# Optimization experiments

Hardware: AMD Instinct MI355X
Metric: run time of the kernel (lower is better)

## Reference

```python
import jax, jax.numpy as jnp
import numpy as np

B, S, F, OWN, H, E = 16384, 37, 17, 9, 256, 128
NOUT = 7 + 16


def setup_inputs() -> dict:
    key = jax.random.key(0)
    ks = jax.random.split(key, 22)
    obs = jax.random.normal(ks[0], (B, S + 1, F), dtype=jnp.float32)
    pad = jax.random.bernoulli(ks[1], 0.3, (B, S))
    obs = obs.at[:, 1:, :].multiply(jnp.where(pad, 0.0, 1.0)[:, :, None])

    def init(k, shape):
        return jax.random.normal(k, shape, dtype=jnp.float32) * 0.05

    params = dict(
        sW1=init(ks[2], (F, H)), sb1=jnp.zeros((H,), jnp.float32),
        sW2=init(ks[3], (H, H)), sb2=jnp.zeros((H,), jnp.float32),
        sW3=init(ks[4], (H, E)), sb3=jnp.zeros((E,), jnp.float32),
        aW1=init(ks[5], (E + OWN, H)), ab1=jnp.zeros((H,), jnp.float32),
        aW2=init(ks[6], (H, H)), ab2=jnp.zeros((H,), jnp.float32),
        aW3=init(ks[7], (H, NOUT)), ab3=jnp.zeros((NOUT,), jnp.float32),
        vW1=init(ks[8], (E + OWN, H)), vb1=jnp.zeros((H,), jnp.float32),
        vW2=init(ks[9], (H, H)), vb2=jnp.zeros((H,), jnp.float32),
        vW3=init(ks[10], (H, 1)), vb3=jnp.zeros((1,), jnp.float32),
    )
    return {"obs": obs, **params}


def reference(obs, sW1, sb1, sW2, sb2, sW3, sb3,
              aW1, ab1, aW2, ab2, aW3, ab3,
              vW1, vb1, vW2, vb2, vW3, vb3):
    s_own = obs[:, 0, :OWN]                      # [B, 9]
    seqs = obs[:, 1:, :]                         # [B, 37, 17]
    # non-padded mask: rows whose abs-sum is nonzero
    mask = (jnp.sum(jnp.abs(seqs), axis=-1) != 0).astype(obs.dtype)  # [B, 37]

    # shared MLP applied to every row; masked positions zeroed before the
    # pooling sum (equivalent to gather->MLP->scatter into zeros->sum)
    h = jax.nn.relu(seqs @ sW1 + sb1)
    h = jax.nn.relu(h @ sW2 + sb2)
    h = jax.nn.relu(h @ sW3 + sb3)               # [B, 37, E]
    h = h * mask[..., None]
    summed = jnp.sum(h, axis=1)                  # [B, E]

    cat = jnp.concatenate([summed, s_own], axis=1)  # [B, E+9]

    a = jax.nn.relu(cat @ aW1 + ab1)
    a = jax.nn.relu(a @ aW2 + ab2)
    action_logits = a @ aW3 + ab3                # [B, 23]

    v = jax.nn.relu(cat @ vW1 + vb1)
    v = jax.nn.relu(v @ vW2 + vb2)
    value = (v @ vW3 + vb3).reshape(-1)          # [B]

    return action_logits, value
```

## Files before the change

### kernel.cpp

```cpp
#include <hip/hip_runtime.h>
#include <hip/hip_bf16.h>

#define B_    16384
#define S_    37
#define F_    17
#define OWN_  9
#define NOUT_ 23
#define OBS_ROW 646

typedef __bf16 bf16x8 __attribute__((ext_vector_type(8)));
typedef __bf16 bf16x4 __attribute__((ext_vector_type(4)));
typedef float  f32x4  __attribute__((ext_vector_type(4)));

#define MFMA(a,b,c) __builtin_amdgcn_mfma_f32_16x16x32_bf16(a, b, c, 0, 0, 0)

#define W1F_OFF   0
#define W2F_OFF   8192
#define W3F_OFF   73728
#define AW1F_OFF  106496
#define AW2F_OFF  147456
#define AW3F_OFF  212992
#define VW1F_OFF  221184
#define VW2F_OFF  262144
#define VW3F_OFF  327680
#define PREP_TOTAL 331776

__global__ void prep_kernel(const float* __restrict__ sW1, const float* __restrict__ sW2,
                            const float* __restrict__ sW3, const float* __restrict__ aW1,
                            const float* __restrict__ aW2, const float* __restrict__ aW3,
                            const float* __restrict__ vW1, const float* __restrict__ vW2,
                            const float* __restrict__ vW3, __bf16* __restrict__ ws)
{
    int j = blockIdx.x * 256 + threadIdx.x;
    const float* src; __bf16* dst; int Np, Ks, Ns;
    if (j < 8192)                  { dst = ws + W1F_OFF;  src = sW1; Np = 256; Ks = 17;  Ns = 256; }
    else if ((j -= 8192)  < 65536) { dst = ws + W2F_OFF;  src = sW2; Np = 256; Ks = 256; Ns = 256; }
    else if ((j -= 65536) < 32768) { dst = ws + W3F_OFF;  src = sW3; Np = 128; Ks = 256; Ns = 128; }
    else if ((j -= 32768) < 40960) { dst = ws + AW1F_OFF; src = aW1; Np = 256; Ks = 137; Ns = 256; }
    else if ((j -= 40960) < 65536) { dst = ws + AW2F_OFF; src = aW2; Np = 256; Ks = 256; Ns = 256; }
    else if ((j -= 65536) < 8192)  { dst = ws + AW3F_OFF; src = aW3; Np = 32;  Ks = 256; Ns = 23;  }
    else if ((j -= 8192)  < 40960) { dst = ws + VW1F_OFF; src = vW1; Np = 256; Ks = 137; Ns = 256; }
    else if ((j -= 40960) < 65536) { dst = ws + VW2F_OFF; src = vW2; Np = 256; Ks = 256; Ns = 256; }
    else { j -= 65536;               dst = ws + VW3F_OFF; src = vW3; Np = 16;  Ks = 256; Ns = 1;   }
    const int c = j / (Np * 8), rem = j - c * Np * 8, n = rem >> 3, e = rem & 7, k = c * 8 + e;
    const float v = (k < Ks && n < Ns) ? src[k * Ns + n] : 0.f;
    dst[j] = (__bf16)v;
}

__global__ __launch_bounds__(512, 2) void fused_kernel(
    const float* __restrict__ obs,
    const float* __restrict__ sb1, const float* __restrict__ sb2, const float* __restrict__ sb3,
    const float* __restrict__ ab1, const float* __restrict__ ab2, const float* __restrict__ ab3,
    const float* __restrict__ vb1, const float* __restrict__ vb2, const float* __restrict__ vb3,
    const __bf16* __restrict__ ws, float* __restrict__ out)
{
    __shared__ __align__(16) char pool[109056];
    __bf16* act1    = (__bf16*)pool;
    __bf16* act2    = (__bf16*)(pool + 32768);
    __bf16* xs_full = (__bf16*)(pool + 65536);
    float*  sm_full = (float*)(pool + 106496);
    __bf16* catf    = (__bf16*)(pool + 65536);
    float*  partial = (float*)pool;

    const __bf16* W1f  = ws + W1F_OFF;
    const __bf16* W2f  = ws + W2F_OFF;
    const __bf16* W3f  = ws + W3F_OFF;
    const __bf16* AW1f = ws + AW1F_OFF;
    const __bf16* AW2f = ws + AW2F_OFF;
    const __bf16* AW3f = ws + AW3F_OFF;
    const __bf16* VW1f = ws + VW1F_OFF;
    const __bf16* VW2f = ws + VW2F_OFF;
    const __bf16* VW3f = ws + VW3F_OFF;

    const int tid  = threadIdx.x;
    const int wave = tid >> 6;
    const int lane = tid & 63;
    const int q    = lane >> 4;
    const int l16  = lane & 15;
    const int qh   = q >> 1;
    const int e4   = (q & 1) * 4;
    const int b0   = blockIdx.x * 16;
    const int nc   = wave & 3;
    const int mr   = wave >> 2;
    const f32x4 z4 = {0.f, 0.f, 0.f, 0.f};

    #pragma unroll
    for (int i = 0; i < 5; ++i)
        ((f32x4*)xs_full)[tid + i * 512] = z4;

    bf16x8 w1f[2], w2f[8][2], w3f[2][8];
    f32x4 b1q[2], b2q[2], b3q[2];
    #pragma unroll
    for (int nt = 0; nt < 2; ++nt) {
        const int n = wave * 32 + nt * 16 + l16;
        w1f[nt] = *(const bf16x8*)(W1f + ((size_t)q * 256 + n) * 8);
        b1q[nt] = *(const f32x4*)(sb1 + wave * 32 + nt * 16 + q * 4);
        b2q[nt] = *(const f32x4*)(sb2 + wave * 32 + nt * 16 + q * 4);
        b3q[nt] = *(const f32x4*)(sb3 + nc * 32 + nt * 16 + q * 4);
        #pragma unroll
        for (int k = 0; k < 8; ++k) {
            w2f[k][nt] = *(const bf16x8*)(W2f + ((size_t)(k * 4 + q) * 256 + n) * 8);
            w3f[nt][k] = *(const bf16x8*)(W3f + ((size_t)(k * 4 + q) * 128 + nc * 32 + nt * 16 + l16) * 8);
        }
    }

    __syncthreads();

    for (int rr = tid; rr < 640; rr += 512) {
        const int g = rr >> 6, tr = rr & 63, b = tr & 15, sl = tr >> 4;
        const int s = g * 4 + sl;
        float sm = 0.f;
        if (s < S_) {
            const float* p = obs + (size_t)(b0 + b) * OBS_ROW + (s + 1) * F_;
            #pragma unroll
            for (int c = 0; c < F_; ++c) {
                const float v = p[c];
                sm += fabsf(v);
                xs_full[g * 2048 + ((c >> 3) * 64 + tr) * 8 + (c & 7)] = (__bf16)v;
            }
        }
        sm_full[rr] = sm;
    }

    __syncthreads();

    f32x4 vsum[2] = {z4, z4};

    for (int it = 0; it < 10; ++it) {
        const __bf16* xg  = xs_full + it * 2048;
        const float*  smg = sm_full + it * 64;

        #pragma unroll
        for (int m = 0; m < 4; ++m) {
            const bf16x8 xm = *(const bf16x8*)(xg + (q * 64 + m * 16 + l16) * 8);
            #pragma unroll
            for (int nt = 0; nt < 2; ++nt) {
                const f32x4 h = MFMA(w1f[nt], xm, z4);
                float v0 = h[0] + b1q[nt][0]; v0 = v0 > 0.f ? v0 : 0.f;
                float v1 = h[1] + b1q[nt][1]; v1 = v1 > 0.f ? v1 : 0.f;
                float v2 = h[2] + b1q[nt][2]; v2 = v2 > 0.f ? v2 : 0.f;
                float v3 = h[3] + b1q[nt][3]; v3 = v3 > 0.f ? v3 : 0.f;
                const bf16x4 pk = {(__bf16)v0, (__bf16)v1, (__bf16)v2, (__bf16)v3};
                *(bf16x4*)(act1 + ((wave * 4 + nt * 2 + qh) * 64 + m * 16 + l16) * 8 + e4) = pk;
            }
        }
        __syncthreads();

        {
            f32x4 h2[2][4];
            #pragma unroll
            for (int nt = 0; nt < 2; ++nt)
                #pragma unroll
                for (int m = 0; m < 4; ++m) h2[nt][m] = z4;
            #pragma unroll
            for (int k = 0; k < 8; ++k) {
                const int k8 = k * 4 + q;
                #pragma unroll
                for (int m = 0; m < 4; ++m) {
                    const bf16x8 a = *(const bf16x8*)(act1 + (k8 * 64 + m * 16 + l16) * 8);
                    h2[0][m] = MFMA(w2f[k][0], a, h2[0][m]);
                    h2[1][m] = MFMA(w2f[k][1], a, h2[1][m]);
                }
            }
            #pragma unroll
            for (int nt = 0; nt < 2; ++nt)
                #pragma unroll
                for (int m = 0; m < 4; ++m) {
                    float v0 = h2[nt][m][0] + b2q[nt][0]; v0 = v0 > 0.f ? v0 : 0.f;
                    float v1 = h2[nt][m][1] + b2q[nt][1]; v1 = v1 > 0.f ? v1 : 0.f;
                    float v2 = h2[nt][m][2] + b2q[nt][2]; v2 = v2 > 0.f ? v2 : 0.f;
                    float v3 = h2[nt][m][3] + b2q[nt][3]; v3 = v3 > 0.f ? v3 : 0.f;
                    const bf16x4 pk = {(__bf16)v0, (__bf16)v1, (__bf16)v2, (__bf16)v3};
                    *(bf16x4*)(act2 + ((wave * 4 + nt * 2 + qh) * 64 + m * 16 + l16) * 8 + e4) = pk;
                }
        }
        __syncthreads();

        {
            f32x4 h3[2][2] = {{z4, z4}, {z4, z4}};
            #pragma unroll
            for (int k = 0; k < 8; ++k) {
                const int k8 = k * 4 + q;
                #pragma unroll
                for (int mi = 0; mi < 2; ++mi) {
                    const bf16x8 a = *(const bf16x8*)(act2 + (k8 * 64 + (mr * 2 + mi) * 16 + l16) * 8);
                    h3[0][mi] = MFMA(w3f[0][k], a, h3[0][mi]);
                    h3[1][mi] = MFMA(w3f[1][k], a, h3[1][mi]);
                }
            }
            #pragma unroll
            for (int mi = 0; mi < 2; ++mi) {
                const float mk = (smg[(mr * 2 + mi) * 16 + l16] != 0.f) ? 1.f : 0.f;
                #pragma unroll
                for (int nt = 0; nt < 2; ++nt)
                    #pragma unroll
                    for (int r = 0; r < 4; ++r) {
                        float v = h3[nt][mi][r] + b3q[nt][r];
                        v = v > 0.f ? v : 0.f;
                        vsum[nt][r] += mk * v;
                    }
            }
        }
    }

    if (mr == 0) {
        #pragma unroll
        for (int nt = 0; nt < 2; ++nt)
            #pragma unroll
            for (int r = 0; r < 4; ++r)
                partial[(nc * 32 + nt * 16 + q * 4 + r) * 16 + l16] = vsum[nt][r];
    }
    if (tid < 16) {
        const float* p = obs + (size_t)(b0 + tid) * OBS_ROW;
        #pragma unroll
        for (int c = 0; c < 8; ++c) catf[(16 * 16 + tid) * 8 + c] = (__bf16)p[c];
        catf[(17 * 16 + tid) * 8 + 0] = (__bf16)p[8];
        #pragma unroll
        for (int c = 1; c < 8; ++c) catf[(17 * 16 + tid) * 8 + c] = (__bf16)0.f;
    } else if (tid < 32) {
        const int rr = tid - 16;
        #pragma unroll
        for (int c = 0; c < 8; ++c) {
            catf[(18 * 16 + rr) * 8 + c] = (__bf16)0.f;
            catf[(19 * 16 + rr) * 8 + c] = (__bf16)0.f;
        }
    }
    __syncthreads();

    if (mr == 1) {
        #pragma unroll
        for (int nt = 0; nt < 2; ++nt) {
            f32x4 t = vsum[nt];
            #pragma unroll
            for (int r = 0; r < 4; ++r)
                t[r] += partial[(nc * 32 + nt * 16 + q * 4 + r) * 16 + l16];
            const bf16x4 pk = {(__bf16)t[0], (__bf16)t[1], (__bf16)t[2], (__bf16)t[3]};
            *(bf16x4*)(catf + ((nc * 4 + nt * 2 + qh) * 16 + l16) * 8 + e4) = pk;
        }
    }
    __syncthreads();

    {
        f32x4 ha[2] = {z4, z4}, hv[2] = {z4, z4};
        #pragma unroll
        for (int k = 0; k < 5; ++k) {
            const int k8 = k * 4 + q;
            const bf16x8 ca = *(const bf16x8*)(catf + (k8 * 16 + l16) * 8);
            #pragma unroll
            for (int nt = 0; nt < 2; ++nt) {
                const int n = wave * 32 + nt * 16 + l16;
                const bf16x8 ba = *(const bf16x8*)(AW1f + ((size_t)k8 * 256 + n) * 8);
                const bf16x8 bv = *(const bf16x8*)(VW1f + ((size_t)k8 * 256 + n) * 8);
                ha[nt] = MFMA(ba, ca, ha[nt]);
                hv[nt] = MFMA(bv, ca, hv[nt]);
            }
        }
        #pragma unroll
        for (int nt = 0; nt < 2; ++nt) {
            const f32x4 ab_ = *(const f32x4*)(ab1 + wave * 32 + nt * 16 + q * 4);
            const f32x4 vb_ = *(const f32x4*)(vb1 + wave * 32 + nt * 16 + q * 4);
            float a0 = ha[nt][0] + ab_[0]; a0 = a0 > 0.f ? a0 : 0.f;
            float a1 = ha[nt][1] + ab_[1]; a1 = a1 > 0.f ? a1 : 0.f;
            float a2 = ha[nt][2] + ab_[2]; a2 = a2 > 0.f ? a2 : 0.f;
            float a3 = ha[nt][3] + ab_[3]; a3 = a3 > 0.f ? a3 : 0.f;
            float u0 = hv[nt][0] + vb_[0]; u0 = u0 > 0.f ? u0 : 0.f;
            float u1 = hv[nt][1] + vb_[1]; u1 = u1 > 0.f ? u1 : 0.f;
            float u2 = hv[nt][2] + vb_[2]; u2 = u2 > 0.f ? u2 : 0.f;
            float u3 = hv[nt][3] + vb_[3]; u3 = u3 > 0.f ? u3 : 0.f;
            const bf16x4 pa = {(__bf16)a0, (__bf16)a1, (__bf16)a2, (__bf16)a3};
            const bf16x4 pv = {(__bf16)u0, (__bf16)u1, (__bf16)u2, (__bf16)u3};
            const int c = wave * 4 + nt * 2 + qh;
            *(bf16x4*)(act1 + (c * 64 + l16) * 8 + e4)      = pa;
            *(bf16x4*)(act1 + (c * 64 + 16 + l16) * 8 + e4) = pv;
        }
    }
    __syncthreads();

    {
        f32x4 ha[2] = {z4, z4}, hv[2] = {z4, z4};
        #pragma unroll
        for (int k = 0; k < 8; ++k) {
            const int k8 = k * 4 + q;
            const bf16x8 a0 = *(const bf16x8*)(act1 + (k8 * 64 + l16) * 8);
            const bf16x8 a1 = *(const bf16x8*)(act1 + (k8 * 64 + 16 + l16) * 8);
            #pragma unroll
            for (int nt = 0; nt < 2; ++nt) {
                const int n = wave * 32 + nt * 16 + l16;
                const bf16x8 ba = *(const bf16x8*)(AW2f + ((size_t)k8 * 256 + n) * 8);
                const bf16x8 bv = *(const bf16x8*)(VW2f + ((size_t)k8 * 256 + n) * 8);
                ha[nt] = MFMA(ba, a0, ha[nt]);
                hv[nt] = MFMA(bv, a1, hv[nt]);
            }
        }
        #pragma unroll
        for (int nt = 0; nt < 2; ++nt) {
            const f32x4 ab_ = *(const f32x4*)(ab2 + wave * 32 + nt * 16 + q * 4);
            const f32x4 vb_ = *(const f32x4*)(vb2 + wave * 32 + nt * 16 + q * 4);
            float a0 = ha[nt][0] + ab_[0]; a0 = a0 > 0.f ? a0 : 0.f;
            float a1 = ha[nt][1] + ab_[1]; a1 = a1 > 0.f ? a1 : 0.f;
            float a2 = ha[nt][2] + ab_[2]; a2 = a2 > 0.f ? a2 : 0.f;
            float a3 = ha[nt][3] + ab_[3]; a3 = a3 > 0.f ? a3 : 0.f;
            float u0 = hv[nt][0] + vb_[0]; u0 = u0 > 0.f ? u0 : 0.f;
            float u1 = hv[nt][1] + vb_[1]; u1 = u1 > 0.f ? u1 : 0.f;
            float u2 = hv[nt][2] + vb_[2]; u2 = u2 > 0.f ? u2 : 0.f;
            float u3 = hv[nt][3] + vb_[3]; u3 = u3 > 0.f ? u3 : 0.f;
            const bf16x4 pa = {(__bf16)a0, (__bf16)a1, (__bf16)a2, (__bf16)a3};
            const bf16x4 pv = {(__bf16)u0, (__bf16)u1, (__bf16)u2, (__bf16)u3};
            const int c = wave * 4 + nt * 2 + qh;
            *(bf16x4*)(act2 + (c * 64 + l16) * 8 + e4)      = pa;
            *(bf16x4*)(act2 + (c * 64 + 16 + l16) * 8 + e4) = pv;
        }
    }
    __syncthreads();

    if (wave < 2) {
        f32x4 acc = z4;
        #pragma unroll
        for (int k = 0; k < 8; ++k) {
            const int k8 = k * 4 + q;
            const bf16x8 a0 = *(const bf16x8*)(act2 + (k8 * 64 + l16) * 8);
            const bf16x8 bf = *(const bf16x8*)(AW3f + ((size_t)k8 * 32 + wave * 16 + l16) * 8);
            acc = MFMA(bf, a0, acc);
        }
        const int nb = wave * 16 + q * 4;
        #pragma unroll
        for (int r = 0; r < 4; ++r) {
            const int n = nb + r;
            if (n < NOUT_)
                out[(size_t)(b0 + l16) * NOUT_ + n] = acc[r] + ab3[n];
        }
    } else if (wave == 2) {
        f32x4 acc = z4;
        #pragma unroll
        for (int k = 0; k < 8; ++k) {
            const int k8 = k * 4 + q;
            const bf16x8 a1 = *(const bf16x8*)(act2 + (k8 * 64 + 16 + l16) * 8);
            const bf16x8 bf = *(const bf16x8*)(VW3f + ((size_t)k8 * 16 + l16) * 8);
            acc = MFMA(bf, a1, acc);
        }
        if (q == 0)
            out[(size_t)B_ * NOUT_ + b0 + l16] = acc[0] + vb3[0];
    }
}

extern "C" void kernel_launch(void* const* d_in, const int* in_sizes, int n_in,
                              void* d_out, int out_size, void* d_ws, size_t ws_size,
                              hipStream_t stream)
{
    const float* obs = (const float*)d_in[0];
    const float* sW1 = (const float*)d_in[1];
    const float* sb1 = (const float*)d_in[2];
    const float* sW2 = (const float*)d_in[3];
    const float* sb2 = (const float*)d_in[4];
    const float* sW3 = (const float*)d_in[5];
    const float* sb3 = (const float*)d_in[6];
    const float* aW1 = (const float*)d_in[7];
    const float* ab1 = (const float*)d_in[8];
    const float* aW2 = (const float*)d_in[9];
    const float* ab2 = (const float*)d_in[10];
    const float* aW3 = (const float*)d_in[11];
    const float* ab3 = (const float*)d_in[12];
    const float* vW1 = (const float*)d_in[13];
    const float* vb1 = (const float*)d_in[14];
    const float* vW2 = (const float*)d_in[15];
    const float* vb2 = (const float*)d_in[16];
    const float* vW3 = (const float*)d_in[17];
    const float* vb3 = (const float*)d_in[18];

    __bf16* ws = (__bf16*)d_ws;
    float* out = (float*)d_out;

    hipLaunchKernelGGL(prep_kernel, dim3(PREP_TOTAL / 256), dim3(256), 0, stream,
                       sW1, sW2, sW3, aW1, aW2, aW3, vW1, vW2, vW3, ws);
    hipLaunchKernelGGL(fused_kernel, dim3(B_ / 16), dim3(512), 0, stream,
                       obs, sb1, sb2, sb3, ab1, ab2, ab3, vb1, vb2, vb3,
                       (const __bf16*)ws, out);
}
```

Measured before the change: 265.8 us.

## Double-buffer obs staging with 128-row tiles and vectorize weight prep

The sequence loop now handles 128 rows (8 slots × 16 batch) per iteration in 5 iterations instead of 64 rows in 10. The next tile's obs values are loaded into registers before the layer-1 MFMAs and written to a second LDS buffer after the first barrier, so global loads overlap compute and the up-front staging of the whole sequence goes away. Obs reads are spread over 4 threads per row, with a shuffle reduction for the padding mask. The prep kernel now writes packed bf16x8 per thread. LDS use grows to about 145 KB, which may limit how many 512-thread blocks fit per CU despite launch_bounds(512,2).

Result: slower. 349.3 us (+31.4%).

```diff
diff --git a/kernel.cpp b/kernel.cpp
--- a/kernel.cpp
+++ b/kernel.cpp
@@ -23,7 +23,7 @@
 #define VW1F_OFF  221184
 #define VW2F_OFF  262144
 #define VW3F_OFF  327680
-#define PREP_TOTAL 331776
+#define PREP_TOTAL8 41472
 
 __global__ void prep_kernel(const float* __restrict__ sW1, const float* __restrict__ sW2,
                             const float* __restrict__ sW3, const float* __restrict__ aW1,
@@ -31,20 +31,26 @@
                             const float* __restrict__ vW1, const float* __restrict__ vW2,
                             const float* __restrict__ vW3, __bf16* __restrict__ ws)
 {
-    int j = blockIdx.x * 256 + threadIdx.x;
+    int j8 = blockIdx.x * 256 + threadIdx.x;
     const float* src; __bf16* dst; int Np, Ks, Ns;
-    if (j < 8192)                  { dst = ws + W1F_OFF;  src = sW1; Np = 256; Ks = 17;  Ns = 256; }
-    else if ((j -= 8192)  < 65536) { dst = ws + W2F_OFF;  src = sW2; Np = 256; Ks = 256; Ns = 256; }
-    else if ((j -= 65536) < 32768) { dst = ws + W3F_OFF;  src = sW3; Np = 128; Ks = 256; Ns = 128; }
-    else if ((j -= 32768) < 40960) { dst = ws + AW1F_OFF; src = aW1; Np = 256; Ks = 137; Ns = 256; }
-    else if ((j -= 40960) < 65536) { dst = ws + AW2F_OFF; src = aW2; Np = 256; Ks = 256; Ns = 256; }
-    else if ((j -= 65536) < 8192)  { dst = ws + AW3F_OFF; src = aW3; Np = 32;  Ks = 256; Ns = 23;  }
-    else if ((j -= 8192)  < 40960) { dst = ws + VW1F_OFF; src = vW1; Np = 256; Ks = 137; Ns = 256; }
-    else if ((j -= 40960) < 65536) { dst = ws + VW2F_OFF; src = vW2; Np = 256; Ks = 256; Ns = 256; }
-    else { j -= 65536;               dst = ws + VW3F_OFF; src = vW3; Np = 16;  Ks = 256; Ns = 1;   }
-    const int c = j / (Np * 8), rem = j - c * Np * 8, n = rem >> 3, e = rem & 7, k = c * 8 + e;
-    const float v = (k < Ks && n < Ns) ? src[k * Ns + n] : 0.f;
-    dst[j] = (__bf16)v;
+    if (j8 < 1024)                { dst = ws + W1F_OFF;  src = sW1; Np = 256; Ks = 17;  Ns = 256; }
+    else if ((j8 -= 1024) < 8192) { dst = ws + W2F_OFF;  src = sW2; Np = 256; Ks = 256; Ns = 256; }
+    else if ((j8 -= 8192) < 4096) { dst = ws + W3F_OFF;  src = sW3; Np = 128; Ks = 256; Ns = 128; }
+    else if ((j8 -= 4096) < 5120) { dst = ws + AW1F_OFF; src = aW1; Np = 256; Ks = 137; Ns = 256; }
+    else if ((j8 -= 5120) < 8192) { dst = ws + AW2F_OFF; src = aW2; Np = 256; Ks = 256; Ns = 256; }
+    else if ((j8 -= 8192) < 1024) { dst = ws + AW3F_OFF; src = aW3; Np = 32;  Ks = 256; Ns = 23;  }
+    else if ((j8 -= 1024) < 5120) { dst = ws + VW1F_OFF; src = vW1; Np = 256; Ks = 137; Ns = 256; }
+    else if ((j8 -= 5120) < 8192) { dst = ws + VW2F_OFF; src = vW2; Np = 256; Ks = 256; Ns = 256; }
+    else { j8 -= 8192;              dst = ws + VW3F_OFF; src = vW3; Np = 16;  Ks = 256; Ns = 1;   }
+    const int c = j8 / Np, n = j8 - c * Np;
+    bf16x8 pk;
+    #pragma unroll
+    for (int e = 0; e < 8; ++e) {
+        const int k = c * 8 + e;
+        const float v = (k < Ks && n < Ns) ? src[k * Ns + n] : 0.f;
+        pk[e] = (__bf16)v;
+    }
+    *(bf16x8*)(dst + (size_t)j8 * 8) = pk;
 }
 
 __global__ __launch_bounds__(512, 2) void fused_kernel(
@@ -54,12 +60,14 @@
     const float* __restrict__ vb1, const float* __restrict__ vb2, const float* __restrict__ vb3,
     const __bf16* __restrict__ ws, float* __restrict__ out)
 {
-    __shared__ __align__(16) char pool[109056];
-    __bf16* act1    = (__bf16*)pool;
-    __bf16* act2    = (__bf16*)(pool + 32768);
-    __bf16* xs_full = (__bf16*)(pool + 65536);
-    float*  sm_full = (float*)(pool + 106496);
-    __bf16* catf    = (__bf16*)(pool + 65536);
+    __shared__ __align__(16) char pool[148480];
+    __bf16* act1 = (__bf16*)pool;
+    __bf16* act2 = (__bf16*)(pool + 65536);
+    __bf16* xs0  = (__bf16*)(pool + 131072);
+    __bf16* xs1  = (__bf16*)(pool + 139264);
+    float*  sm0  = (float*)(pool + 147456);
+    float*  sm1  = (float*)(pool + 147968);
+    __bf16* catf = (__bf16*)(pool + 131072);
     float*  partial = (float*)pool;
 
     const __bf16* W1f  = ws + W1F_OFF;
@@ -84,9 +92,16 @@
     const int mr   = wave >> 2;
     const f32x4 z4 = {0.f, 0.f, 0.f, 0.f};
 
+    const int sr  = tid >> 2;
+    const int sp  = tid & 3;
+    const int sb  = sr & 15;
+    const int ssl = sr >> 4;
+    const int nf  = (sp == 3) ? 5 : 4;
+    const float* obs_row = obs + (size_t)(b0 + sb) * OBS_ROW;
+
     #pragma unroll
-    for (int i = 0; i < 5; ++i)
-        ((f32x4*)xs_full)[tid + i * 512] = z4;
+    for (int i = 0; i < 2; ++i)
+        ((f32x4*)xs0)[tid + i * 512] = z4;
 
     bf16x8 w1f[2], w2f[8][2], w3f[2][8];
     f32x4 b1q[2], b2q[2], b3q[2];
@@ -106,33 +121,45 @@
 
     __syncthreads();
 
-    for (int rr = tid; rr < 640; rr += 512) {
-        const int g = rr >> 6, tr = rr & 63, b = tr & 15, sl = tr >> 4;
-        const int s = g * 4 + sl;
-        float sm = 0.f;
-        if (s < S_) {
-            const float* p = obs + (size_t)(b0 + b) * OBS_ROW + (s + 1) * F_;
-            #pragma unroll
-            for (int c = 0; c < F_; ++c) {
-                const float v = p[c];
-                sm += fabsf(v);
-                xs_full[g * 2048 + ((c >> 3) * 64 + tr) * 8 + (c & 7)] = (__bf16)v;
-            }
-        }
-        sm_full[rr] = sm;
-    }
-
+    {
+        const float* p = obs_row + (ssl + 1) * F_ + sp * 4;
+        float psum = 0.f;
+        #pragma unroll
+        for (int f = 0; f < 5; ++f) {
+            if (f < nf) {
+                const float v = p[f];
+                psum += fabsf(v);
+                const int c = sp * 4 + f;
+                xs0[((c >> 3) * 128 + sr) * 8 + (c & 7)] = (__bf16)v;
+            }
+        }
+        psum += __shfl_xor(psum, 1);
+        psum += __shfl_xor(psum, 2);
+        if (sp == 0) sm0[sr] = psum;
+    }
     __syncthreads();
 
     f32x4 vsum[2] = {z4, z4};
 
-    for (int it = 0; it < 10; ++it) {
-        const __bf16* xg  = xs_full + it * 2048;
-        const float*  smg = sm_full + it * 64;
-
-        #pragma unroll
-        for (int m = 0; m < 4; ++m) {
-            const bf16x8 xm = *(const bf16x8*)(xg + (q * 64 + m * 16 + l16) * 8);
+    for (int it = 0; it < 5; ++it) {
+        __bf16* xc  = (it & 1) ? xs1 : xs0;
+        __bf16* xn  = (it & 1) ? xs0 : xs1;
+        float*  smc = (it & 1) ? sm1 : sm0;
+        float*  smn = (it & 1) ? sm0 : sm1;
+
+        const int s_nx = (it + 1) * 8 + ssl;
+        const bool st_valid = (it < 4) && (s_nx < S_);
+        float stv[5];
+        if (st_valid) {
+            const float* p = obs_row + (s_nx + 1) * F_ + sp * 4;
+            #pragma unroll
+            for (int f = 0; f < 5; ++f)
+                if (f < nf) stv[f] = p[f];
+        }
+
+        #pragma unroll
+        for (int m = 0; m < 8; ++m) {
+            const bf16x8 xm = *(const bf16x8*)(xc + (q * 128 + m * 16 + l16) * 8);
             #pragma unroll
             for (int nt = 0; nt < 2; ++nt) {
                 const f32x4 h = MFMA(w1f[nt], xm, z4);
@@ -141,12 +168,31 @@
                 float v2 = h[2] + b1q[nt][2]; v2 = v2 > 0.f ? v2 : 0.f;
                 float v3 = h[3] + b1q[nt][3]; v3 = v3 > 0.f ? v3 : 0.f;
                 const bf16x4 pk = {(__bf16)v0, (__bf16)v1, (__bf16)v2, (__bf16)v3};
-                *(bf16x4*)(act1 + ((wave * 4 + nt * 2 + qh) * 64 + m * 16 + l16) * 8 + e4) = pk;
+                *(bf16x4*)(act1 + ((wave * 4 + nt * 2 + qh) * 128 + m * 16 + l16) * 8 + e4) = pk;
             }
         }
         __syncthreads();
 
-        {
+        if (it < 4) {
+            float psum = 0.f;
+            if (st_valid) {
+                #pragma unroll
+                for (int f = 0; f < 5; ++f) {
+                    if (f < nf) {
+                        const float v = stv[f];
+                        psum += fabsf(v);
+                        const int c = sp * 4 + f;
+                        xn[((c >> 3) * 128 + sr) * 8 + (c & 7)] = (__bf16)v;
+                    }
+                }
+            }
+            psum += __shfl_xor(psum, 1);
+            psum += __shfl_xor(psum, 2);
+            if (sp == 0) smn[sr] = st_valid ? psum : 0.f;
+        }
+
+        #pragma unroll
+        for (int mh = 0; mh < 2; ++mh) {
             f32x4 h2[2][4];
             #pragma unroll
             for (int nt = 0; nt < 2; ++nt)
@@ -157,7 +203,7 @@
                 const int k8 = k * 4 + q;
                 #pragma unroll
                 for (int m = 0; m < 4; ++m) {
-                    const bf16x8 a = *(const bf16x8*)(act1 + (k8 * 64 + m * 16 + l16) * 8);
+                    const bf16x8 a = *(const bf16x8*)(act1 + (k8 * 128 + mh * 64 + m * 16 + l16) * 8);
                     h2[0][m] = MFMA(w2f[k][0], a, h2[0][m]);
                     h2[1][m] = MFMA(w2f[k][1], a, h2[1][m]);
                 }
@@ -171,35 +217,30 @@
                     float v2 = h2[nt][m][2] + b2q[nt][2]; v2 = v2 > 0.f ? v2 : 0.f;
                     float v3 = h2[nt][m][3] + b2q[nt][3]; v3 = v3 > 0.f ? v3 : 0.f;
                     const bf16x4 pk = {(__bf16)v0, (__bf16)v1, (__bf16)v2, (__bf16)v3};
-                    *(bf16x4*)(act2 + ((wave * 4 + nt * 2 + qh) * 64 + m * 16 + l16) * 8 + e4) = pk;
+                    *(bf16x4*)(act2 + ((wave * 4 + nt * 2 + qh) * 128 + mh * 64 + m * 16 + l16) * 8 + e4) = pk;
                 }
         }
         __syncthreads();
 
-        {
-            f32x4 h3[2][2] = {{z4, z4}, {z4, z4}};
+        #pragma unroll
+        for (int mi = 0; mi < 4; ++mi) {
+            f32x4 h3[2] = {z4, z4};
             #pragma unroll
             for (int k = 0; k < 8; ++k) {
                 const int k8 = k * 4 + q;
+                const bf16x8 a = *(const bf16x8*)(act2 + (k8 * 128 + mr * 64 + mi * 16 + l16) * 8);
+                h3[0] = MFMA(w3f[0][k], a, h3[0]);
+                h3[1] = MFMA(w3f[1][k], a, h3[1]);
+            }
+            const float mv = smc[mr * 64 + mi * 16 + l16];
+            #pragma unroll
+            for (int nt = 0; nt < 2; ++nt)
                 #pragma unroll
-                for (int mi = 0; mi < 2; ++mi) {
-                    const bf16x8 a = *(const bf16x8*)(act2 + (k8 * 64 + (mr * 2 + mi) * 16 + l16) * 8);
-                    h3[0][mi] = MFMA(w3f[0][k], a, h3[0][mi]);
-                    h3[1][mi] = MFMA(w3f[1][k], a, h3[1][mi]);
+                for (int r = 0; r < 4; ++r) {
+                    float v = h3[nt][r] + b3q[nt][r];
+                    v = v > 0.f ? v : 0.f;
+                    vsum[nt][r] += (mv != 0.f) ? v : 0.f;
                 }
-            }
-            #pragma unroll
-            for (int mi = 0; mi < 2; ++mi) {
-                const float mk = (smg[(mr * 2 + mi) * 16 + l16] != 0.f) ? 1.f : 0.f;
-                #pragma unroll
-                for (int nt = 0; nt < 2; ++nt)
-                    #pragma unroll
-                    for (int r = 0; r < 4; ++r) {
-                        float v = h3[nt][mi][r] + b3q[nt][r];
-                        v = v > 0.f ? v : 0.f;
-                        vsum[nt][r] += mk * v;
-                    }
-            }
         }
     }
 
@@ -270,8 +311,8 @@
             const bf16x4 pa = {(__bf16)a0, (__bf16)a1, (__bf16)a2, (__bf16)a3};
             const bf16x4 pv = {(__bf16)u0, (__bf16)u1, (__bf16)u2, (__bf16)u3};
             const int c = wave * 4 + nt * 2 + qh;
-            *(bf16x4*)(act1 + (c * 64 + l16) * 8 + e4)      = pa;
-            *(bf16x4*)(act1 + (c * 64 + 16 + l16) * 8 + e4) = pv;
+            *(bf16x4*)(act1 + (c * 128 + l16) * 8 + e4)      = pa;
+            *(bf16x4*)(act1 + (c * 128 + 16 + l16) * 8 + e4) = pv;
         }
     }
     __syncthreads();
@@ -281,8 +322,8 @@
         #pragma unroll
         for (int k = 0; k < 8; ++k) {
             const int k8 = k * 4 + q;
-            const bf16x8 a0 = *(const bf16x8*)(act1 + (k8 * 64 + l16) * 8);
-            const bf16x8 a1 = *(const bf16x8*)(act1 + (k8 * 64 + 16 + l16) * 8);
+            const bf16x8 a0 = *(const bf16x8*)(act1 + (k8 * 128 + l16) * 8);
+            const bf16x8 a1 = *(const bf16x8*)(act1 + (k8 * 128 + 16 + l16) * 8);
             #pragma unroll
             for (int nt = 0; nt < 2; ++nt) {
                 const int n = wave * 32 + nt * 16 + l16;
@@ -307,8 +348,8 @@
             const bf16x4 pa = {(__bf16)a0, (__bf16)a1, (__bf16)a2, (__bf16)a3};
             const bf16x4 pv = {(__bf16)u0, (__bf16)u1, (__bf16)u2, (__bf16)u3};
             const int c = wave * 4 + nt * 2 + qh;
-            *(bf16x4*)(act2 + (c * 64 + l16) * 8 + e4)      = pa;
-            *(bf16x4*)(act2 + (c * 64 + 16 + l16) * 8 + e4) = pv;
+            *(bf16x4*)(act2 + (c * 128 + l16) * 8 + e4)      = pa;
+            *(bf16x4*)(act2 + (c * 128 + 16 + l16) * 8 + e4) = pv;
         }
     }
     __syncthreads();
@@ -318,7 +359,7 @@
         #pragma unroll
         for (int k = 0; k < 8; ++k) {
             const int k8 = k * 4 + q;
-            const bf16x8 a0 = *(const bf16x8*)(act2 + (k8 * 64 + l16) * 8);
+            const bf16x8 a0 = *(const bf16x8*)(act2 + (k8 * 128 + l16) * 8);
             const bf16x8 bf = *(const bf16x8*)(AW3f + ((size_t)k8 * 32 + wave * 16 + l16) * 8);
             acc = MFMA(bf, a0, acc);
         }
@@ -334,7 +375,7 @@
         #pragma unroll
         for (int k = 0; k < 8; ++k) {
             const int k8 = k * 4 + q;
-            const bf16x8 a1 = *(const bf16x8*)(act2 + (k8 * 64 + 16 + l16) * 8);
+            const bf16x8 a1 = *(const bf16x8*)(act2 + (k8 * 128 + 16 + l16) * 8);
             const bf16x8 bf = *(const bf16x8*)(VW3f + ((size_t)k8 * 16 + l16) * 8);
             acc = MFMA(bf, a1, acc);
         }
@@ -370,7 +411,7 @@
     __bf16* ws = (__bf16*)d_ws;
     float* out = (float*)d_out;
 
-    hipLaunchKernelGGL(prep_kernel, dim3(PREP_TOTAL / 256), dim3(256), 0, stream,
+    hipLaunchKernelGGL(prep_kernel, dim3(PREP_TOTAL8 / 256), dim3(256), 0, stream,
                        sW1, sW2, sW3, aW1, aW2, aW3, vW1, vW2, vW3, ws);
     hipLaunchKernelGGL(fused_kernel, dim3(B_ / 16), dim3(512), 0, stream,
                        obs, sb1, sb2, sb3, ab1, ab2, ab3, vb1, vb2, vb3,
```
